# Kernel tuning notes

Measured on AMD Instinct MI355X. Metric: run time of the kernel, lower is better.

## Reference

```python
import jax, jax.numpy as jnp
import numpy as np

B, S, D = 2, 2048, 1024   # batch, seq, token_dim
H, E = 16, 64             # heads, embedding_size per head


def setup_inputs() -> dict:
    key = jax.random.key(0)
    ks = jax.random.split(key, 5)
    x = jax.random.normal(ks[0], (B, S, D), dtype=jnp.float32)
    attention_mask = jnp.ones((B, S), dtype=jnp.int32)  # accepted but unused, as in source
    # torch.rand -> uniform [0,1)
    w_queries = jax.random.uniform(ks[1], (H, D, E), dtype=jnp.float32)
    w_keys = jax.random.uniform(ks[2], (H, D, E), dtype=jnp.float32)
    w_values = jax.random.uniform(ks[3], (H, D, E), dtype=jnp.float32)
    w_agg = jax.random.uniform(ks[4], (H * E, D), dtype=jnp.float32)
    return {"x": x, "attention_mask": attention_mask, "w_queries": w_queries,
            "w_keys": w_keys, "w_values": w_values, "w_agg": w_agg}


def reference(x, attention_mask, w_queries, w_keys, w_values, w_agg):
    # Batched over all heads at once (original loops in Python per head).
    q = jnp.einsum('bsd,hde->bhse', x, w_queries)  # [B,H,S,E]
    k = jnp.einsum('bsd,hde->bhse', x, w_keys)
    v = jnp.einsum('bsd,hde->bhse', x, w_values)
    scores = jnp.einsum('bhse,bhte->bhst', q, k) / jnp.sqrt(jnp.float32(E))  # [B,H,S,S]
    # NOTE: source applies softmax over dim=1 of the per-head [B,S,S] scores,
    # i.e. over the QUERY axis (axis=2 here), not the usual key axis.
    attn = jax.nn.softmax(scores, axis=2)
    heads = jnp.einsum('bhst,bhte->bhse', attn, v)  # [B,H,S,E]
    # concat along last dim in head order -> [B,S,H*E]
    multi = jnp.transpose(heads, (0, 2, 1, 3)).reshape(B, S, H * E)
    return multi @ w_agg  # [B,S,D]
```

## Files before the change

### kernel.cpp

```cpp
#include <hip/hip_runtime.h>
#include <hip/hip_bf16.h>


typedef __attribute__((ext_vector_type(8))) short bf16x8;
typedef __attribute__((ext_vector_type(4))) float f32x4;

#define C1 0.18033688011112042f

__device__ __forceinline__ unsigned short f2bf(float f){
  union { __hip_bfloat16 h; unsigned short u; } cv;
  cv.h = __float2bfloat16(f);
  return cv.u;
}
__device__ __forceinline__ unsigned int pk2(float a, float b){
  union { __hip_bfloat162 h; unsigned int u; } cv;
  cv.h = __float22bfloat162_rn(make_float2(a, b));
  return cv.u;
}
__device__ __forceinline__ unsigned long long pack4(float a, float b, float c, float d){
  return (unsigned long long)pk2(a, b) | ((unsigned long long)pk2(c, d) << 32);
}
__device__ __forceinline__ float bf2f(unsigned short u){
  unsigned int x = ((unsigned int)u) << 16;
  return __builtin_bit_cast(float, x);
}

__device__ __forceinline__ void swap32(unsigned a, unsigned b, unsigned &x, unsigned &y){
#if __has_builtin(__builtin_amdgcn_permlane32_swap)
  auto r = __builtin_amdgcn_permlane32_swap(a, b, false, false);
  x = r[0]; y = r[1];
#else
  int lane = threadIdx.x & 63;
  unsigned as = __shfl_xor((int)a, 32), bs = __shfl_xor((int)b, 32);
  x = (lane & 32) ? bs : a;
  y = (lane & 32) ? b : as;
#endif
}
__device__ __forceinline__ void swap16(unsigned a, unsigned b, unsigned &x, unsigned &y){
#if __has_builtin(__builtin_amdgcn_permlane16_swap)
  auto r = __builtin_amdgcn_permlane16_swap(a, b, false, false);
  x = r[0]; y = r[1];
#else
  int lane = threadIdx.x & 63;
  unsigned as = __shfl_xor((int)a, 16), bs = __shfl_xor((int)b, 16);
  x = (lane & 16) ? bs : a;
  y = (lane & 16) ? b : as;
#endif
}

#define GLOAD16(SRC, DST)                                                        \
  __builtin_amdgcn_global_load_lds(                                              \
      (const __attribute__((address_space(1))) void*)(SRC),                      \
      (__attribute__((address_space(3))) void*)(DST), 16, 0, 0)

__global__ __launch_bounds__(256) void k_prep(const float* __restrict__ x,
                                              const float* __restrict__ wq,
                                              const float* __restrict__ wk,
                                              const float* __restrict__ wv,
                                              const float* __restrict__ wagg,
                                              unsigned short* __restrict__ Xb,
                                              unsigned short* __restrict__ Wall,
                                              unsigned short* __restrict__ Wat){
  __shared__ unsigned short T[64][72];
  int bid = blockIdx.x;
  if (bid < 4096){
    int i = (bid * 256 + threadIdx.x) * 4;
    float4 v = *reinterpret_cast<const float4*>(x + i);
    *reinterpret_cast<unsigned long long*>(Xb + i) = pack4(v.x, v.y, v.z, v.w);
    return;
  }
  bid -= 4096;
  const int r = threadIdx.x >> 2, c0 = (threadIdx.x & 3) << 4;
  if (bid < 768){
    const int z = bid >> 8, rem = bid & 255, hy = rem >> 4, dt = rem & 15;
    const float* w = ((z == 0) ? wq : ((z == 1) ? wk : wv)) + ((size_t)hy << 16);
    const int d0 = dt * 64;
    const float* src = w + ((size_t)(d0 + r) << 6) + c0;
#pragma unroll
    for (int i = 0; i < 4; ++i){
      float4 v = *(const float4*)(src + 4 * i);
      T[r][c0 + 4 * i + 0] = f2bf(v.x);
      T[r][c0 + 4 * i + 1] = f2bf(v.y);
      T[r][c0 + 4 * i + 2] = f2bf(v.z);
      T[r][c0 + 4 * i + 3] = f2bf(v.w);
    }
    __syncthreads();
    const int e = threadIdx.x >> 2, k0 = (threadIdx.x & 3) << 4;
    union { unsigned short s[8]; bf16x8 v; } u0, u1;
#pragma unroll
    for (int k = 0; k < 8; ++k){ u0.s[k] = T[k0 + k][e]; u1.s[k] = T[k0 + 8 + k][e]; }
    unsigned short* dst = Wall + ((size_t)z << 20) + (((size_t)hy * 64 + e) << 10) + d0 + k0;
    *(bf16x8*)dst = u0.v;
    *(bf16x8*)(dst + 8) = u1.v;
    return;
  }
  bid -= 768;
  {
    const int het = bid >> 4, dt = bid & 15;
    const int d0 = dt * 64, he0 = het * 64;
    const float* src = wagg + ((size_t)(he0 + r) << 10) + d0 + c0;
#pragma unroll
    for (int i = 0; i < 4; ++i){
      float4 v = *(const float4*)(src + 4 * i);
      T[r][c0 + 4 * i + 0] = f2bf(v.x);
      T[r][c0 + 4 * i + 1] = f2bf(v.y);
      T[r][c0 + 4 * i + 2] = f2bf(v.z);
      T[r][c0 + 4 * i + 3] = f2bf(v.w);
    }
    __syncthreads();
    const int d = threadIdx.x >> 2, k0 = (threadIdx.x & 3) << 4;
    union { unsigned short s[8]; bf16x8 v; } u0, u1;
#pragma unroll
    for (int k = 0; k < 8; ++k){ u0.s[k] = T[k0 + k][d]; u1.s[k] = T[k0 + 8 + k][d]; }
    unsigned short* dst = Wat + ((size_t)(d0 + d) << 11) + he0 + k0;
    *(bf16x8*)dst = u0.v;
    *(bf16x8*)(dst + 8) = u1.v;
    *(bf16x8*)(dst + 1024) = u0.v;
    *(bf16x8*)(dst + 1032) = u1.v;
  }
}

__global__ __launch_bounds__(256) void k_proj(const unsigned short* __restrict__ Wall,
                                              const unsigned short* __restrict__ Xb,
                                              unsigned short* __restrict__ Qb,
                                              unsigned short* __restrict__ Kb,
                                              unsigned short* __restrict__ Vt){
  __shared__ __align__(16) unsigned short lds[2][2][4096];
  const int bid = blockIdx.x;
  const int xcd = bid & 7, i = bid >> 3;
  const int yi = i & 3, rest = i >> 2;
  const int xb = rest & 7, z = rest >> 3;
  const int y = xcd + 8 * yi;
  const unsigned short* Wt = Wall + ((size_t)z << 20);
  const int t = threadIdx.x;
  const int w = t >> 6, lane = t & 63, g = lane >> 4, cl = lane & 15;
  const int wn = w >> 1, wm = w & 1;
  const int n0 = xb * 128, m0 = y * 128;

  const int rowS = t & 127;
  const unsigned short* sA = Wt + (size_t)(n0 + rowS) * 1024 + (t >> 7) * 8;
  const unsigned short* sB = Xb + (size_t)(m0 + rowS) * 1024 + (t >> 7) * 8;

  f32x4 acc[4][4];
#pragma unroll
  for (int i2 = 0; i2 < 4; ++i2)
#pragma unroll
    for (int j = 0; j < 4; ++j) acc[i2][j] = f32x4{0.f, 0.f, 0.f, 0.f};

  GLOAD16(sA,      &lds[0][0][t * 8]);
  GLOAD16(sA + 16, &lds[0][0][t * 8 + 2048]);
  GLOAD16(sB,      &lds[0][1][t * 8]);
  GLOAD16(sB + 16, &lds[0][1][t * 8 + 2048]);
  __syncthreads();

#pragma unroll 2
  for (int kt = 0; kt < 32; ++kt){
    const int cur = kt & 1;
    if (kt < 31){
      const unsigned short* nA = sA + (kt + 1) * 32;
      const unsigned short* nB = sB + (kt + 1) * 32;
      GLOAD16(nA,      &lds[cur ^ 1][0][t * 8]);
      GLOAD16(nA + 16, &lds[cur ^ 1][0][t * 8 + 2048]);
      GLOAD16(nB,      &lds[cur ^ 1][1][t * 8]);
      GLOAD16(nB + 16, &lds[cur ^ 1][1][t * 8 + 2048]);
    }
    const unsigned short* la = &lds[cur][0][g * 1024];
    const unsigned short* lb = &lds[cur][1][g * 1024];
    bf16x8 af[4], bq[4];
#pragma unroll
    for (int i2 = 0; i2 < 4; ++i2) af[i2] = *(const bf16x8*)(la + (wn * 64 + i2 * 16 + cl) * 8);
#pragma unroll
    for (int j = 0; j < 4; ++j) bq[j] = *(const bf16x8*)(lb + (wm * 64 + j * 16 + cl) * 8);
#pragma unroll
    for (int i2 = 0; i2 < 4; ++i2)
#pragma unroll
      for (int j = 0; j < 4; ++j)
        acc[i2][j] = __builtin_amdgcn_mfma_f32_16x16x32_bf16(af[i2], bq[j], acc[i2][j], 0, 0, 0);
    __syncthreads();
  }

  const float scale = (z == 0) ? C1 : 1.f;
#pragma unroll
  for (int i2 = 0; i2 < 4; ++i2)
#pragma unroll
    for (int j = 0; j < 4; ++j)
#pragma unroll
      for (int jj = 0; jj < 4; ++jj) acc[i2][j][jj] *= scale;

  if (z < 2){
    unsigned short* outp = (z == 0) ? Qb : Kb;
#pragma unroll
    for (int i2 = 0; i2 < 4; ++i2)
#pragma unroll
      for (int j = 0; j < 4; ++j){
        int m = m0 + wm * 64 + 16 * j + cl;
        int n = n0 + wn * 64 + 16 * i2 + 4 * g;
        *reinterpret_cast<unsigned long long*>(outp + (size_t)m * 1024 + n) =
            pack4(acc[i2][j][0], acc[i2][j][1], acc[i2][j][2], acc[i2][j][3]);
      }
  } else {
    int b = m0 >> 11;
#pragma unroll
    for (int i2 = 0; i2 < 4; ++i2)
#pragma unroll
      for (int j = 0; j < 4; ++j){
        int c2 = (m0 & 2047) + wm * 64 + 16 * j + cl;
        int nb = b * 1024 + n0 + wn * 64 + 16 * i2 + 4 * g;
#pragma unroll
        for (int jj = 0; jj < 4; ++jj)
          Vt[(size_t)(nb + jj) * 2048 + c2] = f2bf(acc[i2][j][jj]);
      }
  }
}

__global__ __launch_bounds__(256) void k_agg(const unsigned short* __restrict__ Wa,
                                             const unsigned short* __restrict__ Hd,
                                             float* __restrict__ outp){
  __shared__ __align__(16) unsigned short lds[2][6144];
  const int bid = blockIdx.x;
  const int xcd = bid & 7, i = bid >> 3;
  const int xb = i & 15, yi = i >> 4;
  const int y = xcd + 8 * yi;
  const int t = threadIdx.x;
  const int w = t >> 6, lane = t & 63, g = lane >> 4, cl = lane & 15;
  const int wn = w >> 1, wm = w & 1;
  const int n0 = xb * 64, m0 = y * 128;

  const unsigned short* sA  = Wa + (size_t)(n0 + (t & 63)) * 2048 + (t >> 6) * 8;
  const unsigned short* sB1 = Hd + (size_t)(m0 + (t & 127)) * 2048 + (t >> 7) * 8;
  unsigned short* dA0  = &lds[0][0]    + t * 8;
  unsigned short* dB10 = &lds[0][2048] + t * 8;

  f32x4 acc[2][4];
#pragma unroll
  for (int j = 0; j < 2; ++j)
#pragma unroll
    for (int i2 = 0; i2 < 4; ++i2) acc[j][i2] = f32x4{0.f, 0.f, 0.f, 0.f};

  GLOAD16(sA,       dA0);
  GLOAD16(sB1,      dB10);
  GLOAD16(sB1 + 16, dB10 + 2048);
  __syncthreads();

#pragma unroll 2
  for (int kt = 0; kt < 64; ++kt){
    const int cur = kt & 1;
    if (kt < 63){
      const unsigned short* nA = sA  + (kt + 1) * 32;
      const unsigned short* nB = sB1 + (kt + 1) * 32;
      GLOAD16(nA,      dA0  + (cur ^ 1) * 6144);
      GLOAD16(nB,      dB10 + (cur ^ 1) * 6144);
      GLOAD16(nB + 16, dB10 + (cur ^ 1) * 6144 + 2048);
    }
    const unsigned short* la = &lds[cur][0];
    const unsigned short* lb = &lds[cur][2048];
    bf16x8 af[2], bq[4];
#pragma unroll
    for (int j = 0; j < 2; ++j) af[j] = *(const bf16x8*)(la + g * 512 + (wn * 32 + j * 16 + cl) * 8);
#pragma unroll
    for (int i2 = 0; i2 < 4; ++i2) bq[i2] = *(const bf16x8*)(lb + g * 1024 + (wm * 64 + i2 * 16 + cl) * 8);
#pragma unroll
    for (int j = 0; j < 2; ++j)
#pragma unroll
      for (int i2 = 0; i2 < 4; ++i2)
        acc[j][i2] = __builtin_amdgcn_mfma_f32_16x16x32_bf16(af[j], bq[i2], acc[j][i2], 0, 0, 0);
    __syncthreads();
  }
#pragma unroll
  for (int j = 0; j < 2; ++j)
#pragma unroll
    for (int i2 = 0; i2 < 4; ++i2){
      int m = m0 + wm * 64 + 16 * i2 + cl;
      int n = n0 + wn * 32 + 16 * j + 4 * g;
      *reinterpret_cast<f32x4*>(outp + (size_t)m * 1024 + n) = acc[j][i2];
    }
}

__global__ __launch_bounds__(256, 4) void k_stats(const unsigned short* __restrict__ Qb,
                                                  const unsigned short* __restrict__ Kb,
                                                  float* __restrict__ mp,
                                                  float* __restrict__ lp){
  __shared__ __align__(16) unsigned short Qs[2][64][64];
  const int B = blockIdx.x;
  const int xcd = B & 7, rest = B >> 3;
  const int tx = rest & 7, gi = rest >> 3;
  const int grp = xcd + 8 * gi;
  const int bh = grp & 31, z = grp >> 5;
  const int b = bh >> 4, h = bh & 15;
  const int w = threadIdx.x >> 6, lane = threadIdx.x & 63;
  const int g = lane >> 4, cl = lane & 15;
  const int t0 = tx * 256 + w * 64;

  const unsigned short* kp = Kb + (size_t)(b * 2048 + t0 + cl) * 1024 + h * 64 + g * 8;
  bf16x8 a[4][2];
#pragma unroll
  for (int ti = 0; ti < 4; ++ti){
    a[ti][0] = *(const bf16x8*)(kp + (size_t)ti * 16 * 1024);
    a[ti][1] = *(const bf16x8*)(kp + (size_t)ti * 16 * 1024 + 32);
  }

  const int r0 = threadIdx.x >> 3, sl = threadIdx.x & 7;
  const unsigned short* qsrc = Qb + (size_t)(b * 2048 + z * 512 + r0) * 1024 + h * 64
                               + ((sl ^ (r0 & 7)) * 8);
  unsigned short* qdst0 = &Qs[0][0][0] + threadIdx.x * 8;

  const int e0 = (g ^ (cl & 7)) * 8;
  const int e1 = ((g + 4) ^ (cl & 7)) * 8;

  float m[16], l[16];
#pragma unroll
  for (int i = 0; i < 16; ++i){ m[i] = -3.0e38f; l[i] = 0.f; }

  GLOAD16(qsrc,             qdst0);
  GLOAD16(qsrc + 32 * 1024, qdst0 + 2048);
  __syncthreads();
  for (int c = 0; c < 8; ++c){
    const int buf = c & 1;
    if (c < 7){
      const unsigned short* s2 = qsrc + (size_t)(c + 1) * 64 * 1024;
      unsigned short* d2 = qdst0 + (buf ^ 1) * 4096;
      GLOAD16(s2,             d2);
      GLOAD16(s2 + 32 * 1024, d2 + 2048);
    }
#pragma unroll
    for (int st = 0; st < 4; ++st){
      const unsigned short* qrow = &Qs[buf][st * 16 + cl][0];
      bf16x8 b0 = *(const bf16x8*)(qrow + e0);
      bf16x8 b1 = *(const bf16x8*)(qrow + e1);
#pragma unroll
      for (int ti = 0; ti < 4; ++ti){
        f32x4 zz = {0.f, 0.f, 0.f, 0.f};
        f32x4 d = __builtin_amdgcn_mfma_f32_16x16x32_bf16(a[ti][0], b0, zz, 0, 0, 0);
        d = __builtin_amdgcn_mfma_f32_16x16x32_bf16(a[ti][1], b1, d, 0, 0, 0);
#pragma unroll
        for (int j = 0; j < 4; ++j) m[ti * 4 + j] = fmaxf(m[ti * 4 + j], d[j]);
      }
    }
    __syncthreads();
  }
#pragma unroll
  for (int off = 1; off < 16; off <<= 1)
#pragma unroll
    for (int i = 0; i < 16; ++i) m[i] = fmaxf(m[i], __shfl_xor(m[i], off));

  GLOAD16(qsrc,             qdst0);
  GLOAD16(qsrc + 32 * 1024, qdst0 + 2048);
  __syncthreads();
  for (int c = 0; c < 8; ++c){
    const int buf = c & 1;
    if (c < 7){
      const unsigned short* s2 = qsrc + (size_t)(c + 1) * 64 * 1024;
      unsigned short* d2 = qdst0 + (buf ^ 1) * 4096;
      GLOAD16(s2,             d2);
      GLOAD16(s2 + 32 * 1024, d2 + 2048);
    }
#pragma unroll
    for (int st = 0; st < 4; ++st){
      const unsigned short* qrow = &Qs[buf][st * 16 + cl][0];
      bf16x8 b0 = *(const bf16x8*)(qrow + e0);
      bf16x8 b1 = *(const bf16x8*)(qrow + e1);
#pragma unroll
      for (int ti = 0; ti < 4; ++ti){
        f32x4 zz = {0.f, 0.f, 0.f, 0.f};
        f32x4 d = __builtin_amdgcn_mfma_f32_16x16x32_bf16(a[ti][0], b0, zz, 0, 0, 0);
        d = __builtin_amdgcn_mfma_f32_16x16x32_bf16(a[ti][1], b1, d, 0, 0, 0);
#pragma unroll
        for (int j = 0; j < 4; ++j) l[ti * 4 + j] += exp2f(d[j] - m[ti * 4 + j]);
      }
    }
    __syncthreads();
  }
#pragma unroll
  for (int off = 1; off < 16; off <<= 1)
#pragma unroll
    for (int i = 0; i < 16; ++i) l[i] += __shfl_xor(l[i], off);

  if (cl == 0){
    size_t base = ((size_t)z * 32 + bh) * 2048 + t0;
#pragma unroll
    for (int ti = 0; ti < 4; ++ti){
      f32x4 mv = {m[ti * 4 + 0], m[ti * 4 + 1], m[ti * 4 + 2], m[ti * 4 + 3]};
      f32x4 lv = {l[ti * 4 + 0], l[ti * 4 + 1], l[ti * 4 + 2], l[ti * 4 + 3]};
      *(f32x4*)(mp + base + ti * 16 + 4 * g) = mv;
      *(f32x4*)(lp + base + ti * 16 + 4 * g) = lv;
    }
  }
}

__global__ __launch_bounds__(256) void k_svr(const float* __restrict__ mp,
                                             const float* __restrict__ lp,
                                             float* __restrict__ m2,
                                             unsigned short* __restrict__ Vt){
  const int row = blockIdx.x;
  const int b = row >> 10, h = (row >> 6) & 15, ee = row & 63;
  const int bh = b * 16 + h;
  const int t8 = threadIdx.x * 8;
  const size_t base = (size_t)bh * 2048 + t8;

  unsigned short* p = Vt + (size_t)row * 2048 + t8;
  bf16x8 v = *(const bf16x8*)p;
  float rl8[8];
#pragma unroll
  for (int half = 0; half < 2; ++half){
    f32x4 m0v = *(const f32x4*)(mp + base + half * 4);
    f32x4 m1v = *(const f32x4*)(mp + base + 65536 + half * 4);
    f32x4 m2v = *(const f32x4*)(mp + base + 131072 + half * 4);
    f32x4 m3v = *(const f32x4*)(mp + base + 196608 + half * 4);
    f32x4 l0v = *(const f32x4*)(lp + base + half * 4);
    f32x4 l1v = *(const f32x4*)(lp + base + 65536 + half * 4);
    f32x4 l2v = *(const f32x4*)(lp + base + 131072 + half * 4);
    f32x4 l3v = *(const f32x4*)(lp + base + 196608 + half * 4);
    f32x4 mo;
#pragma unroll
    for (int j = 0; j < 4; ++j){
      float m = fmaxf(fmaxf(m0v[j], m1v[j]), fmaxf(m2v[j], m3v[j]));
      float l = l0v[j] * exp2f(m0v[j] - m) + l1v[j] * exp2f(m1v[j] - m)
              + l2v[j] * exp2f(m2v[j] - m) + l3v[j] * exp2f(m3v[j] - m);
      rl8[half * 4 + j] = 1.f / l;
      mo[j] = m;
    }
    if (ee == 0) *(f32x4*)(m2 + base + half * 4) = mo;
  }
  float f[8];
#pragma unroll
  for (int j = 0; j < 8; ++j) f[j] = bf2f((unsigned short)v[j]) * rl8[j];
  unsigned long long* q = (unsigned long long*)p;
  q[0] = pack4(f[0], f[1], f[2], f[3]);
  q[1] = pack4(f[4], f[5], f[6], f[7]);
}

__global__ __launch_bounds__(256, 4) void k_attn(const unsigned short* __restrict__ Qb,
                                                 const unsigned short* __restrict__ Kb,
                                                 const unsigned short* __restrict__ Vt,
                                                 const float* __restrict__ m2,
                                                 unsigned short* __restrict__ Hd){
  __shared__ __align__(16) unsigned short KsL[2 * 64 * 64];
  __shared__ __align__(16) unsigned short VsL[2 * 64 * 64];
  __shared__ __align__(16) float Ms[1024];
  const int B = blockIdx.x;
  const int xcd = B & 7, rest = B >> 3;
  const int sx = rest & 15, gi = rest >> 4;
  const int grp = xcd + 8 * gi;
  const int bh = grp & 31, z = grp >> 5;
  const int b = bh >> 4, h = bh & 15;
  const int lane = threadIdx.x & 63;
  const int g = lane >> 4, cl = lane & 15;
  const int s0w = sx * 128 + (threadIdx.x >> 6) * 32;
  const int tbase = z * 1024;

  {
    int i = threadIdx.x * 4;
    f32x4 mv = *(const f32x4*)(m2 + (size_t)bh * 2048 + tbase + i);
    *(f32x4*)&Ms[i] = f32x4{-mv[0], -mv[1], -mv[2], -mv[3]};
  }

  bf16x8 q[2][2];
#pragma unroll
  for (int ss = 0; ss < 2; ++ss){
    const unsigned short* qp = Qb + (size_t)(b * 2048 + s0w + ss * 16 + cl) * 1024 + h * 64 + g * 8;
    q[ss][0] = *(const bf16x8*)(qp);
    q[ss][1] = *(const bf16x8*)(qp + 32);
  }
  f32x4 acc[4][2];
#pragma unroll
  for (int i = 0; i < 4; ++i)
#pragma unroll
    for (int ss = 0; ss < 2; ++ss) acc[i][ss] = f32x4{0.f, 0.f, 0.f, 0.f};

  const int srow = threadIdx.x >> 3;
  const int sseg = ((threadIdx.x & 7) ^ (srow & 7)) * 8;
  const unsigned short* kStage = Kb + (size_t)(b * 2048 + tbase + srow) * 1024 + h * 64 + sseg;
  const unsigned short* vStage = Vt + (size_t)(b * 1024 + h * 64 + srow) * 2048 + tbase + sseg;
  unsigned short* kDst = &KsL[0] + threadIdx.x * 8;
  unsigned short* vDst = &VsL[0] + threadIdx.x * 8;

  const int eK = (g ^ (cl & 7)) * 8;
  const int eK2 = ((g + 4) ^ (cl & 7)) * 8;

#define ASTAGE(c, buf) {                                                          \
    const unsigned short* ks_ = kStage + (size_t)(c) * 64 * 1024;                 \
    const unsigned short* vs_ = vStage + (c) * 64;                                \
    unsigned short* kd_ = kDst + (buf) * 4096;                                    \
    unsigned short* vd_ = vDst + (buf) * 4096;                                    \
    GLOAD16(ks_,             kd_);                                                \
    GLOAD16(ks_ + 32 * 1024, kd_ + 2048);                                         \
    GLOAD16(vs_,             vd_);                                                \
    GLOAD16(vs_ + (size_t)32 * 2048, vd_ + 2048); }

  ASTAGE(0, 0);
  __syncthreads();

  for (int c = 0; c < 16; ++c){
    const int buf = c & 1;
    if (c < 15) ASTAGE(c + 1, buf ^ 1);
    const unsigned short* Kbuf = &KsL[0] + buf * 4096;
    const unsigned short* Vbuf = &VsL[0] + buf * 4096;
#pragma unroll
    for (int sc = 0; sc < 2; ++sc){
      const unsigned short* kr0 = Kbuf + (sc * 32 + cl) * 64;
      const unsigned short* kr1 = Kbuf + (sc * 32 + 16 + cl) * 64;
      bf16x8 a00 = *(const bf16x8*)(kr0 + eK);
      bf16x8 a01 = *(const bf16x8*)(kr0 + eK2);
      bf16x8 a10 = *(const bf16x8*)(kr1 + eK);
      bf16x8 a11 = *(const bf16x8*)(kr1 + eK2);
      f32x4 ci0 = *(const f32x4*)&Ms[c * 64 + sc * 32 + 4 * g];
      f32x4 ci1 = *(const f32x4*)&Ms[c * 64 + sc * 32 + 16 + 4 * g];

      bf16x8 pb[2];
#pragma unroll
      for (int ss = 0; ss < 2; ++ss){
        __builtin_amdgcn_s_setprio(1);
        f32x4 d0 = __builtin_amdgcn_mfma_f32_16x16x32_bf16(a00, q[ss][0], ci0, 0, 0, 0);
        d0 = __builtin_amdgcn_mfma_f32_16x16x32_bf16(a01, q[ss][1], d0, 0, 0, 0);
        f32x4 d1 = __builtin_amdgcn_mfma_f32_16x16x32_bf16(a10, q[ss][0], ci1, 0, 0, 0);
        d1 = __builtin_amdgcn_mfma_f32_16x16x32_bf16(a11, q[ss][1], d1, 0, 0, 0);
        __builtin_amdgcn_s_setprio(0);
        unsigned w00 = pk2(exp2f(d0[0]), exp2f(d0[1]));
        unsigned w01 = pk2(exp2f(d0[2]), exp2f(d0[3]));
        unsigned w10 = pk2(exp2f(d1[0]), exp2f(d1[1]));
        unsigned w11 = pk2(exp2f(d1[2]), exp2f(d1[3]));
        unsigned sa0, sb0, sa1, sb1, W0, W1, W2, W3;
        swap32(w00, w10, sa0, sb0);
        swap32(w01, w11, sa1, sb1);
        swap16(sa0, sb0, W0, W2);
        swap16(sa1, sb1, W1, W3);
        union { unsigned u[4]; bf16x8 v; } fr;
        fr.u[0] = W0; fr.u[1] = W1; fr.u[2] = W2; fr.u[3] = W3;
        pb[ss] = fr.v;
      }
      __builtin_amdgcn_s_setprio(1);
#pragma unroll
      for (int i = 0; i < 4; ++i){
        bf16x8 av = *(const bf16x8*)(Vbuf + (16 * i + cl) * 64 + ((sc * 4 + g) ^ (cl & 7)) * 8);
        acc[i][0] = __builtin_amdgcn_mfma_f32_16x16x32_bf16(av, pb[0], acc[i][0], 0, 0, 0);
        acc[i][1] = __builtin_amdgcn_mfma_f32_16x16x32_bf16(av, pb[1], acc[i][1], 0, 0, 0);
      }
      __builtin_amdgcn_s_setprio(0);
    }
    __syncthreads();
  }
#undef ASTAGE
#pragma unroll
  for (int i = 0; i < 4; ++i)
#pragma unroll
    for (int ss = 0; ss < 2; ++ss){
      *reinterpret_cast<unsigned long long*>(
          Hd + (size_t)(b * 2048 + s0w + ss * 16 + cl) * 2048 + z * 1024 + h * 64 + 16 * i + 4 * g) =
          pack4(acc[i][ss][0], acc[i][ss][1], acc[i][ss][2], acc[i][ss][3]);
    }
}

extern "C" void kernel_launch(void* const* d_in, const int* in_sizes, int n_in,
                              void* d_out, int out_size, void* d_ws, size_t ws_size,
                              hipStream_t stream) {
  const float* x    = (const float*)d_in[0];
  const float* wq   = (const float*)d_in[2];
  const float* wk   = (const float*)d_in[3];
  const float* wv   = (const float*)d_in[4];
  const float* wagg = (const float*)d_in[5];
  float* outp = (float*)d_out;

  char* ws = (char*)d_ws;
  unsigned short* Xb  = (unsigned short*)(ws);
  unsigned short* Hd  = (unsigned short*)(ws);
  unsigned short* Wall= (unsigned short*)(ws + 16777216);
  float* mp = (float*)(ws + 16777216);
  float* lp = (float*)(ws + 17825792);
  float* m2 = (float*)(ws + 18874368);
  unsigned short* Wat = (unsigned short*)(ws + 23068672);
  unsigned short* Qb  = (unsigned short*)(ws + 27262976);
  unsigned short* Kb  = (unsigned short*)(ws + 35651584);
  unsigned short* Vt  = (unsigned short*)(ws + 44040192);

  k_prep<<<dim3(5120), dim3(256), 0, stream>>>(x, wq, wk, wv, wagg, Xb, Wall, Wat);

  k_proj<<<dim3(768), dim3(256), 0, stream>>>(Wall, Xb, Qb, Kb, Vt);

  k_stats<<<dim3(1024), dim3(256), 0, stream>>>(Qb, Kb, mp, lp);
  k_svr  <<<dim3(2048), dim3(256), 0, stream>>>(mp, lp, m2, Vt);

  k_attn<<<dim3(1024), dim3(256), 0, stream>>>(Qb, Kb, Vt, m2, Hd);
  k_agg <<<dim3(512),  dim3(256), 0, stream>>>(Wat, Hd, outp);
}
```

Before: 242.7 us.

## Use single-pass online softmax stats and split query axis into eight chunks

The stats kernel used to make two passes over Q, one for the running max and one for the exp-sum. It now computes both in a single online pass with a branchless rescale and merges lanes with a combined max/sum shuffle reduction. The query axis is also split into 8 chunks of 256 instead of 4 of 512, doubling the grid, and the reduction kernel merges 8 partials. This halves the QK^T MFMA work and Q traffic in stats, at the cost of one extra exp per element. It also lowers the launch-bounds occupancy hint, relocates the workspace buffers for the larger partial arrays, and doubles partial-stat traffic.

```diff
diff --git a/kernel.cpp b/kernel.cpp
--- a/kernel.cpp
+++ b/kernel.cpp
@@ -276,7 +276,7 @@
     }
 }
 
-__global__ __launch_bounds__(256, 4) void k_stats(const unsigned short* __restrict__ Qb,
+__global__ __launch_bounds__(256, 2) void k_stats(const unsigned short* __restrict__ Qb,
                                                   const unsigned short* __restrict__ Kb,
                                                   float* __restrict__ mp,
                                                   float* __restrict__ lp){
@@ -300,7 +300,7 @@
   }
 
   const int r0 = threadIdx.x >> 3, sl = threadIdx.x & 7;
-  const unsigned short* qsrc = Qb + (size_t)(b * 2048 + z * 512 + r0) * 1024 + h * 64
+  const unsigned short* qsrc = Qb + (size_t)(b * 2048 + z * 256 + r0) * 1024 + h * 64
                                + ((sl ^ (r0 & 7)) * 8);
   unsigned short* qdst0 = &Qs[0][0][0] + threadIdx.x * 8;
 
@@ -314,9 +314,9 @@
   GLOAD16(qsrc,             qdst0);
   GLOAD16(qsrc + 32 * 1024, qdst0 + 2048);
   __syncthreads();
-  for (int c = 0; c < 8; ++c){
+  for (int c = 0; c < 4; ++c){
     const int buf = c & 1;
-    if (c < 7){
+    if (c < 3){
       const unsigned short* s2 = qsrc + (size_t)(c + 1) * 64 * 1024;
       unsigned short* d2 = qdst0 + (buf ^ 1) * 4096;
       GLOAD16(s2,             d2);
@@ -333,48 +333,29 @@
         f32x4 d = __builtin_amdgcn_mfma_f32_16x16x32_bf16(a[ti][0], b0, zz, 0, 0, 0);
         d = __builtin_amdgcn_mfma_f32_16x16x32_bf16(a[ti][1], b1, d, 0, 0, 0);
 #pragma unroll
-        for (int j = 0; j < 4; ++j) m[ti * 4 + j] = fmaxf(m[ti * 4 + j], d[j]);
+        for (int j = 0; j < 4; ++j){
+          int idx = ti * 4 + j;
+          float dlt = d[j] - m[idx];
+          float e = exp2f(-fabsf(dlt));
+          bool gt = dlt > 0.f;
+          l[idx] = gt ? fmaf(l[idx], e, 1.f) : (l[idx] + e);
+          m[idx] = gt ? d[j] : m[idx];
+        }
       }
     }
     __syncthreads();
   }
 #pragma unroll
-  for (int off = 1; off < 16; off <<= 1)
-#pragma unroll
-    for (int i = 0; i < 16; ++i) m[i] = fmaxf(m[i], __shfl_xor(m[i], off));
-
-  GLOAD16(qsrc,             qdst0);
-  GLOAD16(qsrc + 32 * 1024, qdst0 + 2048);
-  __syncthreads();
-  for (int c = 0; c < 8; ++c){
-    const int buf = c & 1;
-    if (c < 7){
-      const unsigned short* s2 = qsrc + (size_t)(c + 1) * 64 * 1024;
-      unsigned short* d2 = qdst0 + (buf ^ 1) * 4096;
-      GLOAD16(s2,             d2);
-      GLOAD16(s2 + 32 * 1024, d2 + 2048);
-    }
-#pragma unroll
-    for (int st = 0; st < 4; ++st){
-      const unsigned short* qrow = &Qs[buf][st * 16 + cl][0];
-      bf16x8 b0 = *(const bf16x8*)(qrow + e0);
-      bf16x8 b1 = *(const bf16x8*)(qrow + e1);
-#pragma unroll
-      for (int ti = 0; ti < 4; ++ti){
-        f32x4 zz = {0.f, 0.f, 0.f, 0.f};
-        f32x4 d = __builtin_amdgcn_mfma_f32_16x16x32_bf16(a[ti][0], b0, zz, 0, 0, 0);
-        d = __builtin_amdgcn_mfma_f32_16x16x32_bf16(a[ti][1], b1, d, 0, 0, 0);
-#pragma unroll
-        for (int j = 0; j < 4; ++j) l[ti * 4 + j] += exp2f(d[j] - m[ti * 4 + j]);
-      }
-    }
-    __syncthreads();
-  }
-#pragma unroll
-  for (int off = 1; off < 16; off <<= 1)
-#pragma unroll
-    for (int i = 0; i < 16; ++i) l[i] += __shfl_xor(l[i], off);
-
+  for (int off = 1; off < 16; off <<= 1){
+#pragma unroll
+    for (int i = 0; i < 16; ++i){
+      float om = __shfl_xor(m[i], off);
+      float ol = __shfl_xor(l[i], off);
+      float mn = fmaxf(m[i], om);
+      l[i] = l[i] * exp2f(m[i] - mn) + ol * exp2f(om - mn);
+      m[i] = mn;
+    }
+  }
   if (cl == 0){
     size_t base = ((size_t)z * 32 + bh) * 2048 + t0;
 #pragma unroll
@@ -402,24 +383,24 @@
   float rl8[8];
 #pragma unroll
   for (int half = 0; half < 2; ++half){
-    f32x4 m0v = *(const f32x4*)(mp + base + half * 4);
-    f32x4 m1v = *(const f32x4*)(mp + base + 65536 + half * 4);
-    f32x4 m2v = *(const f32x4*)(mp + base + 131072 + half * 4);
-    f32x4 m3v = *(const f32x4*)(mp + base + 196608 + half * 4);
-    f32x4 l0v = *(const f32x4*)(lp + base + half * 4);
-    f32x4 l1v = *(const f32x4*)(lp + base + 65536 + half * 4);
-    f32x4 l2v = *(const f32x4*)(lp + base + 131072 + half * 4);
-    f32x4 l3v = *(const f32x4*)(lp + base + 196608 + half * 4);
-    f32x4 mo;
-#pragma unroll
-    for (int j = 0; j < 4; ++j){
-      float m = fmaxf(fmaxf(m0v[j], m1v[j]), fmaxf(m2v[j], m3v[j]));
-      float l = l0v[j] * exp2f(m0v[j] - m) + l1v[j] * exp2f(m1v[j] - m)
-              + l2v[j] * exp2f(m2v[j] - m) + l3v[j] * exp2f(m3v[j] - m);
-      rl8[half * 4 + j] = 1.f / l;
-      mo[j] = m;
-    }
-    if (ee == 0) *(f32x4*)(m2 + base + half * 4) = mo;
+    f32x4 mm = *(const f32x4*)(mp + base + half * 4);
+#pragma unroll
+    for (int k = 1; k < 8; ++k){
+      f32x4 mk = *(const f32x4*)(mp + base + (size_t)k * 65536 + half * 4);
+#pragma unroll
+      for (int j = 0; j < 4; ++j) mm[j] = fmaxf(mm[j], mk[j]);
+    }
+    f32x4 lsum = {0.f, 0.f, 0.f, 0.f};
+#pragma unroll
+    for (int k = 0; k < 8; ++k){
+      f32x4 mk = *(const f32x4*)(mp + base + (size_t)k * 65536 + half * 4);
+      f32x4 lk = *(const f32x4*)(lp + base + (size_t)k * 65536 + half * 4);
+#pragma unroll
+      for (int j = 0; j < 4; ++j) lsum[j] += lk[j] * exp2f(mk[j] - mm[j]);
+    }
+#pragma unroll
+    for (int j = 0; j < 4; ++j) rl8[half * 4 + j] = 1.f / lsum[j];
+    if (ee == 0) *(f32x4*)(m2 + base + half * 4) = mm;
   }
   float f[8];
 #pragma unroll
@@ -565,8 +546,8 @@
   unsigned short* Hd  = (unsigned short*)(ws);
   unsigned short* Wall= (unsigned short*)(ws + 16777216);
   float* mp = (float*)(ws + 16777216);
-  float* lp = (float*)(ws + 17825792);
-  float* m2 = (float*)(ws + 18874368);
+  float* lp = (float*)(ws + 18874368);
+  float* m2 = (float*)(ws + 20971520);
   unsigned short* Wat = (unsigned short*)(ws + 23068672);
   unsigned short* Qb  = (unsigned short*)(ws + 27262976);
   unsigned short* Kb  = (unsigned short*)(ws + 35651584);
@@ -576,7 +557,7 @@
 
   k_proj<<<dim3(768), dim3(256), 0, stream>>>(Wall, Xb, Qb, Kb, Vt);
 
-  k_stats<<<dim3(1024), dim3(256), 0, stream>>>(Qb, Kb, mp, lp);
+  k_stats<<<dim3(2048), dim3(256), 0, stream>>>(Qb, Kb, mp, lp);
   k_svr  <<<dim3(2048), dim3(256), 0, stream>>>(mp, lp, m2, Vt);
 
   k_attn<<<dim3(1024), dim3(256), 0, stream>>>(Qb, Kb, Vt, m2, Hd);
```

Result: slower. 266.3 us (+9.7%).
